# Performance work log

Measured on AMD Instinct MI355X. Metric: run time of the kernel, lower is better.

The kernel has to match this reference:

```python
import jax, jax.numpy as jnp
import numpy as np
from jax import lax

BN_EPS = 1e-5


def setup_inputs() -> dict:
    key = jax.random.key(0)
    k = jax.random.split(key, 7)
    B, H, W = 128, 224, 224
    return {
        "x": jax.random.normal(k[0], (B, 1, H, W), dtype=jnp.float32),
        "conv_w": jax.random.normal(k[1], (16, 1, 5, 5), dtype=jnp.float32) * 0.1,
        "conv_b": jax.random.normal(k[2], (16,), dtype=jnp.float32) * 0.1,
        "gamma": jax.random.uniform(k[3], (16,), dtype=jnp.float32, minval=0.5, maxval=1.5),
        "beta": jax.random.normal(k[4], (16,), dtype=jnp.float32) * 0.1,
        "run_mean": jax.random.normal(k[5], (16,), dtype=jnp.float32) * 0.1,
        "run_var": jax.random.uniform(k[6], (16,), dtype=jnp.float32, minval=0.5, maxval=1.5),
    }


def reference(x, conv_w, conv_b, gamma, beta, run_mean, run_var):
    # Conv2d(1,16,5,stride=1,padding=2): NCHW x OIHW -> NCHW
    y = lax.conv_general_dilated(
        x, conv_w, window_strides=(1, 1), padding=[(2, 2), (2, 2)],
        dimension_numbers=("NCHW", "OIHW", "NCHW"))
    y = y + conv_b[None, :, None, None]
    # BatchNorm2d(16) in inference form with running stats
    scale = gamma * lax.rsqrt(run_var + BN_EPS)
    y = y * scale[None, :, None, None] + (beta - run_mean * scale)[None, :, None, None]
    # ReLU
    y = jnp.maximum(y, 0.0)
    # MaxPool2d(kernel=2, stride=2)
    out = lax.reduce_window(y, -jnp.inf, lax.max,
                            window_dimensions=(1, 1, 2, 2),
                            window_strides=(1, 1, 2, 2),
                            padding="VALID")
    return out  # [B, 16, H/2, W/2]
```

## Files before the change

### kernel.cpp

```cpp
#include <hip/hip_runtime.h>
#include <stdint.h>

#define IMG 224
#define OUT_DIM 112
#define NCH 16
#define TILE_Y 16
#define R_ROWS 20
#define HJ 116
#define HSZ (R_ROWS * HJ)

typedef _Float16 h8t  __attribute__((ext_vector_type(8)));
typedef float    f32x4 __attribute__((ext_vector_type(4)));
typedef uint32_t u32x4 __attribute__((ext_vector_type(4)));

__global__ __launch_bounds__(256)
void conv_bn_relu_pool(const float* __restrict__ x,
                       const float* __restrict__ conv_w,
                       const float* __restrict__ conv_b,
                       const float* __restrict__ gamma,
                       const float* __restrict__ beta,
                       const float* __restrict__ run_mean,
                       const float* __restrict__ run_var,
                       float* __restrict__ out)
{
    __shared__ uint32_t H[2 * HSZ];

    const int tid = threadIdx.x;
    const int b   = blockIdx.y;
    const int ty  = blockIdx.x * TILE_Y;
    const float* xb = x + (size_t)b * IMG * IMG;

    const int lane = tid & 63;
    const int wv   = tid >> 6;
    const int pp   = lane & 15;
    const int g    = lane >> 4;

    const float* w = conv_w + pp * 25;
    float w0 = w[g*5+0], w1 = w[g*5+1], w2 = w[g*5+2], w3 = w[g*5+3], w4 = w[g*5+4];
    float e0 = (2*g   < 5) ? w[20 + 2*g]     : 0.f;
    float e1 = (2*g+1 < 5) ? w[20 + 2*g + 1] : 0.f;
    u32x4 bu;
    bu[0] = __builtin_bit_cast(uint32_t, __builtin_amdgcn_cvt_pkrtz(w0, w1));
    bu[1] = __builtin_bit_cast(uint32_t, __builtin_amdgcn_cvt_pkrtz(w2, w3));
    bu[2] = __builtin_bit_cast(uint32_t, __builtin_amdgcn_cvt_pkrtz(w4, 0.f));
    bu[3] = __builtin_bit_cast(uint32_t, __builtin_amdgcn_cvt_pkrtz(e0, e1));
    h8t B1 = __builtin_bit_cast(h8t, bu);
    float sc = gamma[pp] * rsqrtf(run_var[pp] + 1e-5f);
    float sh = fmaf(sc, conv_b[pp] - run_mean[pp], beta[pp]);

    for (int i = tid; i < HSZ; i += 256) {
        int r = i / HJ, j = i - r * HJ;
        int gy = ty - 2 + r;
        int c  = 2 * j;
        float v0 = 0.f, v1 = 0.f, v2 = 0.f;
        if ((unsigned)gy < IMG) {
            const float* row = xb + gy * IMG;
            if ((unsigned)(c - 2) < IMG) v0 = row[c - 2];
            if ((unsigned)(c - 1) < IMG) v1 = row[c - 1];
            if ((unsigned)(c    ) < IMG) v2 = row[c];
        }
        H[i]       = __builtin_bit_cast(uint32_t, __builtin_amdgcn_cvt_pkrtz(v0, v1));
        H[HSZ + i] = __builtin_bit_cast(uint32_t, __builtin_amdgcn_cvt_pkrtz(v1, v2));
    }
    __syncthreads();

    const uint32_t* Hq = H + (pp & 1) * HSZ + (pp >> 1);
    float* outb = out + ((size_t)b * NCH + pp) * (OUT_DIM * OUT_DIM);

    #pragma unroll
    for (int s = 0; s < 2; ++s) {
        const int y0 = 4 * wv + 2 * s;
        const int oy = blockIdx.x * 8 + 2 * wv + s;
        const uint32_t* rA = Hq + (y0 + g) * HJ;
        const uint32_t* r4 = Hq + (y0 + 4) * HJ + g;
        float* orow = outb + oy * OUT_DIM + 2 * g;

        #pragma unroll
        for (int sub = 0; sub < 14; ++sub) {
            const int j0 = sub * 8;
            f32x4 accA = {0.f, 0.f, 0.f, 0.f};
            f32x4 accB = {0.f, 0.f, 0.f, 0.f};

            u32x4 a1 = { rA[j0], rA[j0 + 1], rA[j0 + 2], r4[j0] };
            accA = __builtin_amdgcn_mfma_f32_16x16x32_f16(
                       __builtin_bit_cast(h8t, a1), B1, accA, 0, 0, 0);
            u32x4 c1 = { rA[j0 + HJ], rA[j0 + 1 + HJ], rA[j0 + 2 + HJ], r4[j0 + HJ] };
            accB = __builtin_amdgcn_mfma_f32_16x16x32_f16(
                       __builtin_bit_cast(h8t, c1), B1, accB, 0, 0, 0);

            float m0 = fmaxf(fmaxf(accA[0], accA[1]), fmaxf(accB[0], accB[1]));
            float m1 = fmaxf(fmaxf(accA[2], accA[3]), fmaxf(accB[2], accB[3]));
            float y0v = fmaxf(fmaf(m0, sc, sh), 0.f);
            float y1v = fmaxf(fmaf(m1, sc, sh), 0.f);
            *(float2*)(orow + sub * 8) = make_float2(y0v, y1v);
        }
    }
}

extern "C" void kernel_launch(void* const* d_in, const int* in_sizes, int n_in,
                              void* d_out, int out_size, void* d_ws, size_t ws_size,
                              hipStream_t stream) {
    const float* x        = (const float*)d_in[0];
    const float* conv_w   = (const float*)d_in[1];
    const float* conv_b   = (const float*)d_in[2];
    const float* gamma    = (const float*)d_in[3];
    const float* beta     = (const float*)d_in[4];
    const float* run_mean = (const float*)d_in[5];
    const float* run_var  = (const float*)d_in[6];
    float* out = (float*)d_out;

    dim3 grid(IMG / TILE_Y, 128);
    dim3 block(256);
    conv_bn_relu_pool<<<grid, block, 0, stream>>>(
        x, conv_w, conv_b, gamma, beta, run_mean, run_var, out);
}
```

Measured before the change: 153.3 us.

## Vectorize halo staging loads and double tile height per block

The shared-memory staging loop now reads four floats per thread with a 16-byte vector load and writes packed fp16 pairs as 8-byte stores. The left and right padding columns are filled by a separate small pass, and the read pointer is shifted by one to match the new layout. The tile height also doubles from 16 to 32 rows, so each wave computes four output rows instead of two. This cuts per-element global load instructions and the relative halo overhead, at the cost of more shared memory per block and a grid half as tall, which may reduce occupancy.

Result: faster. 148.1 us (-3.3%).

```diff
diff --git a/kernel.cpp b/kernel.cpp
--- a/kernel.cpp
+++ b/kernel.cpp
@@ -4,8 +4,8 @@
 #define IMG 224
 #define OUT_DIM 112
 #define NCH 16
-#define TILE_Y 16
-#define R_ROWS 20
+#define TILE_Y 32
+#define R_ROWS 36
 #define HJ 116
 #define HSZ (R_ROWS * HJ)
 
@@ -23,7 +23,7 @@
                        const float* __restrict__ run_var,
                        float* __restrict__ out)
 {
-    __shared__ uint32_t H[2 * HSZ];
+    __shared__ __align__(16) uint32_t H[2 * HSZ];
 
     const int tid = threadIdx.x;
     const int b   = blockIdx.y;
@@ -48,29 +48,46 @@
     float sc = gamma[pp] * rsqrtf(run_var[pp] + 1e-5f);
     float sh = fmaf(sc, conv_b[pp] - run_mean[pp], beta[pp]);
 
-    for (int i = tid; i < HSZ; i += 256) {
-        int r = i / HJ, j = i - r * HJ;
+    for (int i = tid; i < R_ROWS * 56; i += 256) {
+        int r = i / 56, q = i - r * 56;
         int gy = ty - 2 + r;
-        int c  = 2 * j;
-        float v0 = 0.f, v1 = 0.f, v2 = 0.f;
+        int c  = 4 * q;
+        f32x4 v = {0.f, 0.f, 0.f, 0.f};
+        float v4 = 0.f;
         if ((unsigned)gy < IMG) {
             const float* row = xb + gy * IMG;
-            if ((unsigned)(c - 2) < IMG) v0 = row[c - 2];
-            if ((unsigned)(c - 1) < IMG) v1 = row[c - 1];
-            if ((unsigned)(c    ) < IMG) v2 = row[c];
+            v = *(const f32x4*)(row + c);
+            if (q < 55) v4 = row[c + 4];
         }
-        H[i]       = __builtin_bit_cast(uint32_t, __builtin_amdgcn_cvt_pkrtz(v0, v1));
-        H[HSZ + i] = __builtin_bit_cast(uint32_t, __builtin_amdgcn_cvt_pkrtz(v1, v2));
+        uint32_t* base = H + r * HJ + 2 + (c >> 1);
+        uint2 p0, p1;
+        p0.x = __builtin_bit_cast(uint32_t, __builtin_amdgcn_cvt_pkrtz(v[0], v[1]));
+        p0.y = __builtin_bit_cast(uint32_t, __builtin_amdgcn_cvt_pkrtz(v[2], v[3]));
+        p1.x = __builtin_bit_cast(uint32_t, __builtin_amdgcn_cvt_pkrtz(v[1], v[2]));
+        p1.y = __builtin_bit_cast(uint32_t, __builtin_amdgcn_cvt_pkrtz(v[3], v4));
+        *(uint2*)(base)       = p0;
+        *(uint2*)(base + HSZ) = p1;
+    }
+    if (tid < 2 * R_ROWS) {
+        int pl = tid & 1, r = tid >> 1;
+        int gy = ty - 2 + r;
+        float f0 = 0.f;
+        if (pl == 1 && (unsigned)gy < IMG) f0 = xb[gy * IMG];
+        uint32_t pm1 = __builtin_bit_cast(uint32_t, __builtin_amdgcn_cvt_pkrtz(0.f, f0));
+        uint32_t* row = H + pl * HSZ + r * HJ;
+        row[0] = 0u;
+        row[1] = pl ? pm1 : 0u;
+        *(uint2*)(row + 114) = make_uint2(0u, 0u);
     }
     __syncthreads();
 
-    const uint32_t* Hq = H + (pp & 1) * HSZ + (pp >> 1);
+    const uint32_t* Hq = H + (pp & 1) * HSZ + (pp >> 1) + 1;
     float* outb = out + ((size_t)b * NCH + pp) * (OUT_DIM * OUT_DIM);
 
     #pragma unroll
-    for (int s = 0; s < 2; ++s) {
-        const int y0 = 4 * wv + 2 * s;
-        const int oy = blockIdx.x * 8 + 2 * wv + s;
+    for (int s = 0; s < 4; ++s) {
+        const int y0 = 8 * wv + 2 * s;
+        const int oy = blockIdx.x * 16 + 4 * wv + s;
         const uint32_t* rA = Hq + (y0 + g) * HJ;
         const uint32_t* r4 = Hq + (y0 + 4) * HJ + g;
         float* orow = outb + oy * OUT_DIM + 2 * g;
```
